# Kernel optimization log

Measured on AMD Instinct MI355X. Metric: run time of the kernel, lower is better.

## Reference

```python
import jax, jax.numpy as jnp
import numpy as np


def _prelu(x, a):
    return jnp.where(x >= 0, x, a * x)


def setup_inputs() -> dict:
    key = jax.random.key(0)
    ks = jax.random.split(key, 10)
    B, N, h_dim, H_dim, g_dim, Kc, n = 64, 4096, 256, 1024, 512, 32, 2048
    hs = jax.random.normal(ks[0], (B, N, h_dim), dtype=jnp.float32)
    cs_o = jax.random.randint(ks[1], (B, N), 0, Kc, dtype=jnp.int32)

    def lin(k, fi, fo):
        return jax.random.normal(k, (fi, fo), dtype=jnp.float32) / np.sqrt(fi).astype(np.float32)

    a = jnp.full((1,), 0.25, dtype=jnp.float32)  # torch PReLU default
    return {
        "hs": hs,
        "W1": lin(ks[2], h_dim, H_dim), "b1": jnp.zeros((H_dim,), jnp.float32), "a1": a,
        "W2": lin(ks[3], H_dim, H_dim), "b2": jnp.zeros((H_dim,), jnp.float32), "a2": a,
        "W3": lin(ks[4], H_dim, H_dim), "b3": jnp.zeros((H_dim,), jnp.float32), "a3": a,
        "W4": lin(ks[5], H_dim, H_dim), "b4": jnp.zeros((H_dim,), jnp.float32), "a4": a,
        "W5": lin(ks[6], H_dim, H_dim), "b5": jnp.zeros((H_dim,), jnp.float32), "a5": a,
        "W6": lin(ks[7], H_dim, g_dim), "b6": jnp.zeros((g_dim,), jnp.float32),
        "cs_o": cs_o,
        "n": n,
    }


def reference(hs, W1, b1, a1, W2, b2, a2, W3, b3, a3, W4, b4, a4, W5, b5, a5, W6, b6, cs_o, n):
    B, N, h_dim = hs.shape
    cs = cs_o.at[:, n:].set(-1)                  # points >= n are unassigned
    K = int(jnp.max(cs)) + 1                      # static (concrete data)
    Ks = jnp.max(cs, axis=1)                      # [B] max cluster id per batch entry

    # per-cluster masked sums (vectorized segment-sum over all K at once)
    onehot = (cs[:, :, None] == jnp.arange(K)[None, None, :]).astype(hs.dtype)  # [B,N,K]
    Hk = jnp.einsum('bnk,bnh->bkh', onehot, hs)   # [B,K,h] sum of hs per cluster
    hn = hs[:, n, :]                              # [B,h] the point being assigned
    # H = [H_0..H_{K-1}, H_0+h_n..H_{K-1}+h_n, h_n]
    H = jnp.concatenate([Hk, Hk + hn[:, None, :], hn[:, None, :]], axis=1)  # [B,2K+1,h]

    mk = (jnp.sum(onehot, axis=1) > 0).astype(hs.dtype)  # [B,K] cluster non-empty
    gs_mask = jnp.concatenate([mk, mk, jnp.ones((B, 1), hs.dtype)], axis=1)[:, :, None]

    # 6-layer MLP g applied to all B*(2K+1) rows at once
    x = H.reshape(B * (2 * K + 1), h_dim)
    x = _prelu(x @ W1 + b1, a1)
    x = _prelu(x @ W2 + b2, a2)
    x = _prelu(x @ W3 + b3, a3)
    x = _prelu(x @ W4 + b4, a4)
    x = _prelu(x @ W5 + b5, a5)
    gs = (x @ W6 + b6).reshape(B, 2 * K + 1, -1) * gs_mask  # [B,2K+1,g]

    # G_k = sum_{j<K, j!=k} gs_j + gs_{k+K} ;  G_K = sum_{j<K} gs_j + gs_{2K}
    S = jnp.sum(gs[:, :K], axis=1)                                   # [B,g]
    G_head = (S[:, None, :] - gs[:, :K] + gs[:, K:2 * K]) * mk[:, :, None]
    G_last = S + gs[:, 2 * K]
    G = jnp.concatenate([G_head, G_last[:, None, :]], axis=1)        # [B,K+1,g]

    # per-batch correction: if Ks[b]==k (k<K-1), move G[b,-1] to slot k+1, zero last
    need = (Ks >= 0) & (Ks < K - 1)
    kidx = jnp.arange(K + 1)
    move = need[:, None] & (kidx[None, :] == (Ks + 1)[:, None])      # [B,K+1]
    G = jnp.where(move[:, :, None], G[:, K:K + 1, :], G)
    G = jnp.where((need[:, None] & (kidx[None, :] == K))[:, :, None], 0.0, G)
    G_mask = jnp.where(need[:, None] & (kidx[None, :] >= (Ks + 2)[:, None]),
                       0.0, jnp.ones((B, K + 1), hs.dtype))
    return (G, G_mask)
```

## Files before the change

### kernel.cpp

```cpp
#include <hip/hip_runtime.h>
#include <hip/hip_bf16.h>
#include <stdint.h>

using bf16x8 = __attribute__((ext_vector_type(8))) short;
using f32x4  = __attribute__((ext_vector_type(4))) float;

#define BATCH 64
#define NTOK  4096
#define HD    256
#define HDIM  1024
#define GD    512

__device__ __forceinline__ ushort f2bf(float f) {
  union { __hip_bfloat16 h; ushort u; } cv;
  cv.h = __float2bfloat16(f);
  return cv.u;
}

__device__ __forceinline__ void gload_lds16(const void* gsrc, void* ldst) {
  typedef const __attribute__((address_space(1))) uint32_t* gas_p;
  typedef __attribute__((address_space(3))) uint32_t* las_p;
  __builtin_amdgcn_global_load_lds((gas_p)(uintptr_t)gsrc, (las_p)(uintptr_t)ldst, 16, 0, 0);
}

struct WTArgs {
  const float* src[6];
  ushort* dst[6];
  int fi[6];
  int fo[6];
};

__global__ __launch_bounds__(256) void wtrans_kernel(WTArgs a) {
  int z = blockIdx.z;
  int fi = a.fi[z], fo = a.fo[z];
  int c0 = blockIdx.x * 32;
  int r0 = blockIdx.y * 32;
  if (c0 >= fo || r0 >= fi) return;
  const float* W = a.src[z];
  ushort* Wt = a.dst[z];
  __shared__ float tile[32][33];
  int tx = threadIdx.x & 31, ty = threadIdx.x >> 5;
#pragma unroll
  for (int j = 0; j < 4; ++j)
    tile[ty + j * 8][tx] = W[(size_t)(r0 + ty + j * 8) * fo + (c0 + tx)];
  __syncthreads();
#pragma unroll
  for (int j = 0; j < 4; ++j)
    Wt[(size_t)(c0 + ty + j * 8) * fi + (r0 + tx)] = f2bf(tile[tx][ty + j * 8]);
}

__global__ __launch_bounds__(256) void bucket_kernel(const int* __restrict__ cs,
                                                     const int* __restrict__ nptr,
                                                     int* __restrict__ idx,
                                                     int* __restrict__ off,
                                                     int* __restrict__ cnt,
                                                     int* __restrict__ Ks,
                                                     int K) {
  int b = blockIdx.x, t = threadIdx.x;
  int n = *nptr;
  __shared__ int csb[NTOK];
  __shared__ int hist[256 * 32];
  __shared__ int btot[32];
  __shared__ int bbase[32];
  const int* csrow = cs + (size_t)b * NTOK;
  int mymax = -1;
  for (int i = t; i < n; i += 256) { int v = csrow[i]; csb[i] = v; mymax = max(mymax, v); }
#pragma unroll
  for (int k = 0; k < 32; ++k) hist[t * 32 + k] = 0;
  __syncthreads();
  int chunkN = (n + 255) >> 8;
  for (int c = 0; c < chunkN; ++c) {
    int i = c * 256 + t;
    if (i < n) hist[t * 32 + csb[i]]++;
  }
  __syncthreads();
  if (t < K) {
    int run = 0;
    for (int r = 0; r < 256; ++r) { int tmp = hist[r * 32 + t]; hist[r * 32 + t] = run; run += tmp; }
    btot[t] = run;
  }
  __syncthreads();
  if (t == 0) {
    int base = 0;
    for (int k = 0; k < K; ++k) { bbase[k] = base; base += btot[k]; }
  }
  __syncthreads();
  if (t < K) { off[b * K + t] = bbase[t]; cnt[b * K + t] = btot[t]; }
  int* idxb = idx + (size_t)b * NTOK;
  for (int c = 0; c < chunkN; ++c) {
    int i = c * 256 + t;
    if (i < n) {
      int k = csb[i];
      int s = bbase[k] + hist[t * 32 + k]++;
      idxb[s] = i;
    }
  }
  for (int o2 = 32; o2; o2 >>= 1) mymax = max(mymax, __shfl_down(mymax, o2));
  __shared__ int red[4];
  if ((t & 63) == 0) red[t >> 6] = mymax;
  __syncthreads();
  if (t == 0) {
    int r = red[0];
    for (int i = 1; i < 4; ++i) r = max(r, red[i]);
    Ks[b] = r;
  }
}

__global__ __launch_bounds__(256) void aggregate2_kernel(const float* __restrict__ hs,
                                                         const int* __restrict__ idx,
                                                         const int* __restrict__ off,
                                                         const int* __restrict__ cnt,
                                                         const int* __restrict__ nptr,
                                                         ushort* __restrict__ X,
                                                         int K) {
  int b = blockIdx.x / K, k = blockIdx.x % K;
  int t = threadIdx.x;
  int n = *nptr;
  int c = cnt[b * K + k];
  int o = off[b * K + k];
  const float* hsb = hs + (size_t)b * NTOK * HD;
  const int* ids = idx + (size_t)b * NTOK + o;
  __shared__ int sid[256];
  float a0 = 0.f, a1 = 0.f, a2 = 0.f, a3 = 0.f;
  for (int j0 = 0; j0 < c; j0 += 256) {
    __syncthreads();
    if (j0 + t < c) sid[t] = ids[j0 + t];
    __syncthreads();
    int lim = min(256, c - j0);
    int j = 0;
    for (; j + 3 < lim; j += 4) {
      int i0 = sid[j], i1 = sid[j + 1], i2 = sid[j + 2], i3 = sid[j + 3];
      a0 += hsb[(size_t)i0 * HD + t];
      a1 += hsb[(size_t)i1 * HD + t];
      a2 += hsb[(size_t)i2 * HD + t];
      a3 += hsb[(size_t)i3 * HD + t];
    }
    for (; j < lim; ++j) a0 += hsb[(size_t)sid[j] * HD + t];
  }
  float sum = (a0 + a1) + (a2 + a3);
  float hn = hsb[(size_t)n * HD + t];
  int R = 2 * K + 1;
  X[((size_t)b * R + k) * HD + t]     = f2bf(sum);
  X[((size_t)b * R + K + k) * HD + t] = f2bf(sum + hn);
  if (k == 0) X[((size_t)b * R + 2 * K) * HD + t] = f2bf(hn);
}

template <bool LAST>
__global__ __launch_bounds__(256) void gemm_kernel(const ushort* __restrict__ A,
                                                   const ushort* __restrict__ Bt,
                                                   const float* __restrict__ bias,
                                                   const float* __restrict__ aptr,
                                                   void* __restrict__ Cout,
                                                   int N, int Kd) {
  __shared__ ushort As[2][2][128 * 32];
  __shared__ ushort Bs[2][2][64 * 32];
  int tid = threadIdx.x;
  int lane = tid & 63, w = tid >> 6;
  int wr = w >> 1, wc = w & 1;
  int fr = lane & 15, fq = lane >> 4;

  int nwg = gridDim.x;
  int flat = blockIdx.x;
  int q8 = nwg >> 3, r8 = nwg & 7;
  int xcd = flat & 7, loc = flat >> 3;
  int swz = (xcd < r8 ? xcd * (q8 + 1) : r8 * (q8 + 1) + (xcd - r8) * q8) + loc;
  int NC = N >> 6;
  int brow = swz / NC, bcol = swz % NC;

  size_t row0 = (size_t)brow * 128;
  size_t col0 = (size_t)bcol * 64;

  const ushort* Abase = A + row0 * (size_t)Kd;
  const ushort* Bbase = Bt + col0 * (size_t)Kd;

  f32x4 acc[4][2] = {};

  int qA0 = w * 64 + lane;
  int qA1 = 256 + w * 64 + lane;
  int rA0 = qA0 >> 2, kA0 = (qA0 & 3) * 8;
  int rA1 = qA1 >> 2, kA1 = (qA1 & 3) * 8;
  int rB = qA0 >> 2, kB = (qA0 & 3) * 8;

  auto stage = [&](int buf, int k0) {
#pragma unroll
    for (int h = 0; h < 2; ++h) {
      int kh = k0 + h * 32;
      gload_lds16(Abase + (size_t)rA0 * Kd + kh + kA0, &As[buf][h][(w)     * 512]);
      gload_lds16(Abase + (size_t)rA1 * Kd + kh + kA1, &As[buf][h][(4 + w) * 512]);
      gload_lds16(Bbase + (size_t)rB  * Kd + kh + kB,  &Bs[buf][h][(w)     * 512]);
    }
  };

  int nt = Kd >> 6;
  int cur = 0;
  stage(0, 0);
  __syncthreads();
  for (int t = 0; t < nt; ++t) {
    if (t + 1 < nt) stage(cur ^ 1, (t + 1) * 64);
    bf16x8 af[2][4], bfv[2][2];
#pragma unroll
    for (int h = 0; h < 2; ++h) {
#pragma unroll
      for (int m = 0; m < 4; ++m)
        af[h][m] = *(const bf16x8*)&As[cur][h][(wr * 64 + m * 16 + fr) * 32 + fq * 8];
#pragma unroll
      for (int nn = 0; nn < 2; ++nn)
        bfv[h][nn] = *(const bf16x8*)&Bs[cur][h][(wc * 32 + nn * 16 + fr) * 32 + fq * 8];
    }
#pragma unroll
    for (int h = 0; h < 2; ++h)
#pragma unroll
      for (int m = 0; m < 4; ++m)
#pragma unroll
        for (int nn = 0; nn < 2; ++nn)
          acc[m][nn] = __builtin_amdgcn_mfma_f32_16x16x32_bf16(af[h][m], bfv[h][nn], acc[m][nn], 0, 0, 0);
    __syncthreads();
    cur ^= 1;
  }

  float alpha = 0.f;
  if (!LAST) alpha = aptr[0];
#pragma unroll
  for (int nn = 0; nn < 2; ++nn) {
    size_t col = col0 + wc * 32 + nn * 16 + fr;
    float bv = bias[col];
#pragma unroll
    for (int m = 0; m < 4; ++m) {
      size_t rbase = row0 + wr * 64 + m * 16 + fq * 4;
#pragma unroll
      for (int j = 0; j < 4; ++j) {
        float v = acc[m][nn][j] + bv;
        if (!LAST) {
          v = (v >= 0.f) ? v : alpha * v;
          ((ushort*)Cout)[(rbase + j) * N + col] = f2bf(v);
        } else {
          ((float*)Cout)[(rbase + j) * N + col] = v;
        }
      }
    }
  }
}

__global__ __launch_bounds__(256) void final_kernel(const float* __restrict__ gs,
                                                    const int* __restrict__ counts,
                                                    const int* __restrict__ Ks,
                                                    float* __restrict__ out,
                                                    int K) {
  int b = blockIdx.x, t = threadIdx.x;
  __shared__ float mk[64];
  __shared__ int sks;
  if (t < K) mk[t] = (counts[b * K + t] > 0) ? 1.f : 0.f;
  if (t == 0) sks = Ks[b];
  __syncthreads();
  int ks = sks;
  bool need = (ks >= 0) && (ks < K - 1);
  const float* g = gs + (size_t)b * (2 * K + 1) * GD;
  float S0 = 0.f, S1 = 0.f;
  for (int k = 0; k < K; ++k) {
    S0 += g[(size_t)k * GD + t] * mk[k];
    S1 += g[(size_t)k * GD + t + 256] * mk[k];
  }
  float gl0 = S0 + g[(size_t)(2 * K) * GD + t];
  float gl1 = S1 + g[(size_t)(2 * K) * GD + t + 256];
  float* G  = out + (size_t)b * (K + 1) * GD;
  float* Gm = out + (size_t)BATCH * (K + 1) * GD + (size_t)b * (K + 1);
  for (int kk = 0; kk <= K; ++kk) {
    float v0, v1;
    if (kk == K)                  { v0 = need ? 0.f : gl0; v1 = need ? 0.f : gl1; }
    else if (need && kk == ks + 1){ v0 = gl0;              v1 = gl1; }
    else {
      v0 = mk[kk] * (S0 - g[(size_t)kk * GD + t]       + g[(size_t)(K + kk) * GD + t]);
      v1 = mk[kk] * (S1 - g[(size_t)kk * GD + t + 256] + g[(size_t)(K + kk) * GD + t + 256]);
    }
    G[(size_t)kk * GD + t]       = v0;
    G[(size_t)kk * GD + t + 256] = v1;
  }
  if (t <= K) Gm[t] = (need && t >= ks + 2) ? 0.f : 1.f;
}

extern "C" void kernel_launch(void* const* d_in, const int* in_sizes, int n_in,
                              void* d_out, int out_size, void* d_ws, size_t ws_size,
                              hipStream_t stream) {
  const float* hs = (const float*)d_in[0];
  const float* W[6]  = {(const float*)d_in[1], (const float*)d_in[4], (const float*)d_in[7],
                        (const float*)d_in[10], (const float*)d_in[13], (const float*)d_in[16]};
  const float* bb[6] = {(const float*)d_in[2], (const float*)d_in[5], (const float*)d_in[8],
                        (const float*)d_in[11], (const float*)d_in[14], (const float*)d_in[17]};
  const float* aa[5] = {(const float*)d_in[3], (const float*)d_in[6], (const float*)d_in[9],
                        (const float*)d_in[12], (const float*)d_in[15]};
  const int* cs   = (const int*)d_in[18];
  const int* nptr = (const int*)d_in[19];
  float* out = (float*)d_out;

  int K = out_size / (BATCH * (GD + 1)) - 1;
  int M = BATCH * (2 * K + 1);
  int Mpad = (M + 127) / 128 * 128;

  char* base = (char*)d_ws;
  size_t off_b = 0;
  auto alloc = [&](size_t bytes) {
    char* p = base + off_b;
    off_b = (off_b + bytes + 255) & ~(size_t)255;
    return p;
  };
  ushort* W1t  = (ushort*)alloc((size_t)HDIM * HD * 2);
  ushort* W2t  = (ushort*)alloc((size_t)HDIM * HDIM * 2);
  ushort* W3t  = (ushort*)alloc((size_t)HDIM * HDIM * 2);
  ushort* W4t  = (ushort*)alloc((size_t)HDIM * HDIM * 2);
  ushort* W5bt = (ushort*)alloc((size_t)HDIM * HDIM * 2);
  ushort* W6t  = (ushort*)alloc((size_t)GD * HDIM * 2);
  int* idx     = (int*)alloc((size_t)BATCH * NTOK * 4);
  int* offb    = (int*)alloc((size_t)BATCH * K * 4);
  int* cntb    = (int*)alloc((size_t)BATCH * K * 4);
  int* Ksb     = (int*)alloc(BATCH * 4);
  ushort* X    = (ushort*)alloc((size_t)Mpad * HD * 2);
  ushort* Y0   = (ushort*)alloc((size_t)Mpad * HDIM * 2);
  ushort* Y1   = (ushort*)alloc((size_t)Mpad * HDIM * 2);
  float*  gsb  = (float*)alloc((size_t)Mpad * GD * 4);
  (void)ws_size; (void)n_in; (void)in_sizes;

  WTArgs wa;
  wa.src[0] = W[0]; wa.dst[0] = W1t;  wa.fi[0] = HD;   wa.fo[0] = HDIM;
  wa.src[1] = W[1]; wa.dst[1] = W2t;  wa.fi[1] = HDIM; wa.fo[1] = HDIM;
  wa.src[2] = W[2]; wa.dst[2] = W3t;  wa.fi[2] = HDIM; wa.fo[2] = HDIM;
  wa.src[3] = W[3]; wa.dst[3] = W4t;  wa.fi[3] = HDIM; wa.fo[3] = HDIM;
  wa.src[4] = W[4]; wa.dst[4] = W5bt; wa.fi[4] = HDIM; wa.fo[4] = HDIM;
  wa.src[5] = W[5]; wa.dst[5] = W6t;  wa.fi[5] = HDIM; wa.fo[5] = GD;
  hipLaunchKernelGGL(wtrans_kernel, dim3(32, 32, 6), dim3(256), 0, stream, wa);

  hipLaunchKernelGGL(bucket_kernel, dim3(BATCH), dim3(256), 0, stream, cs, nptr, idx, offb, cntb, Ksb, K);
  hipLaunchKernelGGL(aggregate2_kernel, dim3(BATCH * K), dim3(256), 0, stream, hs, idx, offb, cntb, nptr, X, K);
  hipMemsetAsync(X + (size_t)M * HD, 0, (size_t)(Mpad - M) * HD * 2, stream);

  dim3 blk(256);
  int NR = Mpad / 128;
  hipLaunchKernelGGL((gemm_kernel<false>), dim3(NR * (HDIM / 64)), blk, 0, stream, X,   W1t,  bb[0], aa[0], (void*)Y0, HDIM, HD);
  hipLaunchKernelGGL((gemm_kernel<false>), dim3(NR * (HDIM / 64)), blk, 0, stream, Y0,  W2t,  bb[1], aa[1], (void*)Y1, HDIM, HDIM);
  hipLaunchKernelGGL((gemm_kernel<false>), dim3(NR * (HDIM / 64)), blk, 0, stream, Y1,  W3t,  bb[2], aa[2], (void*)Y0, HDIM, HDIM);
  hipLaunchKernelGGL((gemm_kernel<false>), dim3(NR * (HDIM / 64)), blk, 0, stream, Y0,  W4t,  bb[3], aa[3], (void*)Y1, HDIM, HDIM);
  hipLaunchKernelGGL((gemm_kernel<false>), dim3(NR * (HDIM / 64)), blk, 0, stream, Y1,  W5bt, bb[4], aa[4], (void*)Y0, HDIM, HDIM);
  hipLaunchKernelGGL((gemm_kernel<true>),  dim3(NR * (GD / 64)),   blk, 0, stream, Y0,  W6t,  bb[5], nullptr, (void*)gsb, GD, HDIM);

  hipLaunchKernelGGL(final_kernel, dim3(BATCH), dim3(256), 0, stream, gsb, cntb, Ksb, out, K);
}
```

Measured before the change: 155.4 us.

## Merge preprocessing kernels, vectorize aggregation, triple-buffer GEMM with single barrier

Combines the weight transpose and bucketing into one launch with a flat grid, removing a kernel launch and the wasted empty blocks of the 3D transpose grid. The aggregation kernel now reads float4 rows split across four wavefronts and reduces the partials in shared memory, and it zeroes the padding rows itself so the separate memset goes away. The GEMM moves to a 3-stage LDS ring with explicit vmcnt waits, one barrier per k-step and raised priority around the MFMA block, so global loads are issued two steps ahead. This raises LDS use per GEMM block, which may reduce occupancy.

```diff
diff --git a/kernel.cpp b/kernel.cpp
--- a/kernel.cpp
+++ b/kernel.cpp
@@ -30,79 +30,86 @@
   int fo[6];
 };
 
-__global__ __launch_bounds__(256) void wtrans_kernel(WTArgs a) {
-  int z = blockIdx.z;
-  int fi = a.fi[z], fo = a.fo[z];
-  int c0 = blockIdx.x * 32;
-  int r0 = blockIdx.y * 32;
-  if (c0 >= fo || r0 >= fi) return;
-  const float* W = a.src[z];
-  ushort* Wt = a.dst[z];
-  __shared__ float tile[32][33];
-  int tx = threadIdx.x & 31, ty = threadIdx.x >> 5;
-#pragma unroll
-  for (int j = 0; j < 4; ++j)
-    tile[ty + j * 8][tx] = W[(size_t)(r0 + ty + j * 8) * fo + (c0 + tx)];
-  __syncthreads();
-#pragma unroll
-  for (int j = 0; j < 4; ++j)
-    Wt[(size_t)(c0 + ty + j * 8) * fi + (r0 + tx)] = f2bf(tile[tx][ty + j * 8]);
-}
-
-__global__ __launch_bounds__(256) void bucket_kernel(const int* __restrict__ cs,
-                                                     const int* __restrict__ nptr,
-                                                     int* __restrict__ idx,
-                                                     int* __restrict__ off,
-                                                     int* __restrict__ cnt,
-                                                     int* __restrict__ Ks,
-                                                     int K) {
-  int b = blockIdx.x, t = threadIdx.x;
-  int n = *nptr;
+__global__ __launch_bounds__(256) void pre_kernel(WTArgs a,
+                                                  const int* __restrict__ cs,
+                                                  const int* __restrict__ nptr,
+                                                  int* __restrict__ idx,
+                                                  int* __restrict__ off,
+                                                  int* __restrict__ cnt,
+                                                  int* __restrict__ Ks,
+                                                  int K) {
   __shared__ int csb[NTOK];
   __shared__ int hist[256 * 32];
   __shared__ int btot[32];
   __shared__ int bbase[32];
-  const int* csrow = cs + (size_t)b * NTOK;
-  int mymax = -1;
-  for (int i = t; i < n; i += 256) { int v = csrow[i]; csb[i] = v; mymax = max(mymax, v); }
-#pragma unroll
-  for (int k = 0; k < 32; ++k) hist[t * 32 + k] = 0;
-  __syncthreads();
-  int chunkN = (n + 255) >> 8;
-  for (int c = 0; c < chunkN; ++c) {
-    int i = c * 256 + t;
-    if (i < n) hist[t * 32 + csb[i]]++;
-  }
-  __syncthreads();
-  if (t < K) {
-    int run = 0;
-    for (int r = 0; r < 256; ++r) { int tmp = hist[r * 32 + t]; hist[r * 32 + t] = run; run += tmp; }
-    btot[t] = run;
-  }
-  __syncthreads();
-  if (t == 0) {
-    int base = 0;
-    for (int k = 0; k < K; ++k) { bbase[k] = base; base += btot[k]; }
-  }
-  __syncthreads();
-  if (t < K) { off[b * K + t] = bbase[t]; cnt[b * K + t] = btot[t]; }
-  int* idxb = idx + (size_t)b * NTOK;
-  for (int c = 0; c < chunkN; ++c) {
-    int i = c * 256 + t;
-    if (i < n) {
-      int k = csb[i];
-      int s = bbase[k] + hist[t * 32 + k]++;
-      idxb[s] = i;
-    }
-  }
-  for (int o2 = 32; o2; o2 >>= 1) mymax = max(mymax, __shfl_down(mymax, o2));
-  __shared__ int red[4];
-  if ((t & 63) == 0) red[t >> 6] = mymax;
-  __syncthreads();
-  if (t == 0) {
-    int r = red[0];
-    for (int i = 1; i < 4; ++i) r = max(r, red[i]);
-    Ks[b] = r;
+  __shared__ float tile[32][33];
+  int t = threadIdx.x;
+  if (blockIdx.x < BATCH) {
+    int b = blockIdx.x;
+    int n = *nptr;
+    const int* csrow = cs + (size_t)b * NTOK;
+    int mymax = -1;
+    for (int i = t; i < n; i += 256) { int v = csrow[i]; csb[i] = v; mymax = max(mymax, v); }
+#pragma unroll
+    for (int k = 0; k < 32; ++k) hist[t * 32 + k] = 0;
+    __syncthreads();
+    int chunkN = (n + 255) >> 8;
+    for (int c = 0; c < chunkN; ++c) {
+      int i = c * 256 + t;
+      if (i < n) hist[t * 32 + csb[i]]++;
+    }
+    __syncthreads();
+    if (t < K) {
+      int run = 0;
+      for (int r = 0; r < 256; ++r) { int tmp = hist[r * 32 + t]; hist[r * 32 + t] = run; run += tmp; }
+      btot[t] = run;
+    }
+    __syncthreads();
+    if (t == 0) {
+      int base = 0;
+      for (int k = 0; k < K; ++k) { bbase[k] = base; base += btot[k]; }
+    }
+    __syncthreads();
+    if (t < K) { off[b * K + t] = bbase[t]; cnt[b * K + t] = btot[t]; }
+    int* idxb = idx + (size_t)b * NTOK;
+    for (int c = 0; c < chunkN; ++c) {
+      int i = c * 256 + t;
+      if (i < n) {
+        int k = csb[i];
+        int s = bbase[k] + hist[t * 32 + k]++;
+        idxb[s] = i;
+      }
+    }
+    for (int o2 = 32; o2; o2 >>= 1) mymax = max(mymax, __shfl_down(mymax, o2));
+    if ((t & 63) == 0) btot[16 + (t >> 6)] = mymax;
+    __syncthreads();
+    if (t == 0) {
+      int r = btot[16];
+      for (int i = 1; i < 4; ++i) r = max(r, btot[16 + i]);
+      Ks[b] = r;
+    }
+  } else {
+    int f = blockIdx.x - BATCH;
+    int z = 0;
+    while (true) {
+      int nb = (a.fo[z] >> 5) * (a.fi[z] >> 5);
+      if (f < nb) break;
+      f -= nb; ++z;
+    }
+    int ncx = a.fo[z] >> 5;
+    int cx = f % ncx, cy = f / ncx;
+    int c0 = cx * 32, r0 = cy * 32;
+    int fo = a.fo[z], fi = a.fi[z];
+    const float* W = a.src[z];
+    ushort* Wt = a.dst[z];
+    int tx = t & 31, ty = t >> 5;
+#pragma unroll
+    for (int j = 0; j < 4; ++j)
+      tile[ty + j * 8][tx] = W[(size_t)(r0 + ty + j * 8) * fo + (c0 + tx)];
+    __syncthreads();
+#pragma unroll
+    for (int j = 0; j < 4; ++j)
+      Wt[(size_t)(c0 + ty + j * 8) * fi + (r0 + tx)] = f2bf(tile[tx][ty + j * 8]);
   }
 }
 
@@ -112,37 +119,50 @@
                                                          const int* __restrict__ cnt,
                                                          const int* __restrict__ nptr,
                                                          ushort* __restrict__ X,
-                                                         int K) {
+                                                         int K, int M, int Mpad) {
   int b = blockIdx.x / K, k = blockIdx.x % K;
   int t = threadIdx.x;
+  int g = t >> 6, l = t & 63;
   int n = *nptr;
   int c = cnt[b * K + k];
   int o = off[b * K + k];
   const float* hsb = hs + (size_t)b * NTOK * HD;
   const int* ids = idx + (size_t)b * NTOK + o;
   __shared__ int sid[256];
-  float a0 = 0.f, a1 = 0.f, a2 = 0.f, a3 = 0.f;
+  __shared__ float part[4][HD];
+  float ax = 0.f, ay = 0.f, az = 0.f, aw = 0.f;
+  float bx = 0.f, by = 0.f, bz = 0.f, bw = 0.f;
   for (int j0 = 0; j0 < c; j0 += 256) {
     __syncthreads();
     if (j0 + t < c) sid[t] = ids[j0 + t];
     __syncthreads();
     int lim = min(256, c - j0);
-    int j = 0;
-    for (; j + 3 < lim; j += 4) {
-      int i0 = sid[j], i1 = sid[j + 1], i2 = sid[j + 2], i3 = sid[j + 3];
-      a0 += hsb[(size_t)i0 * HD + t];
-      a1 += hsb[(size_t)i1 * HD + t];
-      a2 += hsb[(size_t)i2 * HD + t];
-      a3 += hsb[(size_t)i3 * HD + t];
-    }
-    for (; j < lim; ++j) a0 += hsb[(size_t)sid[j] * HD + t];
-  }
-  float sum = (a0 + a1) + (a2 + a3);
+    int j = g;
+    for (; j + 4 < lim; j += 8) {
+      float4 v0 = ((const float4*)&hsb[(size_t)sid[j] * HD])[l];
+      float4 v1 = ((const float4*)&hsb[(size_t)sid[j + 4] * HD])[l];
+      ax += v0.x; ay += v0.y; az += v0.z; aw += v0.w;
+      bx += v1.x; by += v1.y; bz += v1.z; bw += v1.w;
+    }
+    for (; j < lim; j += 4) {
+      float4 v = ((const float4*)&hsb[(size_t)sid[j] * HD])[l];
+      ax += v.x; ay += v.y; az += v.z; aw += v.w;
+    }
+  }
+  part[g][l * 4 + 0] = ax + bx;
+  part[g][l * 4 + 1] = ay + by;
+  part[g][l * 4 + 2] = az + bz;
+  part[g][l * 4 + 3] = aw + bw;
+  __syncthreads();
+  float sum = ((part[0][t] + part[1][t]) + (part[2][t] + part[3][t]));
   float hn = hsb[(size_t)n * HD + t];
   int R = 2 * K + 1;
   X[((size_t)b * R + k) * HD + t]     = f2bf(sum);
   X[((size_t)b * R + K + k) * HD + t] = f2bf(sum + hn);
-  if (k == 0) X[((size_t)b * R + 2 * K) * HD + t] = f2bf(hn);
+  if (k == 0) {
+    X[((size_t)b * R + 2 * K) * HD + t] = f2bf(hn);
+    for (int r = M + b; r < Mpad; r += BATCH) X[(size_t)r * HD + t] = 0;
+  }
 }
 
 template <bool LAST>
@@ -152,8 +172,8 @@
                                                    const float* __restrict__ aptr,
                                                    void* __restrict__ Cout,
                                                    int N, int Kd) {
-  __shared__ ushort As[2][2][128 * 32];
-  __shared__ ushort Bs[2][2][64 * 32];
+  __shared__ ushort As[3][2][128 * 32];
+  __shared__ ushort Bs[3][2][64 * 32];
   int tid = threadIdx.x;
   int lane = tid & 63, w = tid >> 6;
   int wr = w >> 1, wc = w & 1;
@@ -192,11 +212,14 @@
   };
 
   int nt = Kd >> 6;
-  int cur = 0;
   stage(0, 0);
-  __syncthreads();
+  stage(1, 64);
   for (int t = 0; t < nt; ++t) {
-    if (t + 1 < nt) stage(cur ^ 1, (t + 1) * 64);
+    if (t + 1 < nt) asm volatile("s_waitcnt vmcnt(6)" ::: "memory");
+    else            asm volatile("s_waitcnt vmcnt(0)" ::: "memory");
+    __builtin_amdgcn_s_barrier();
+    __builtin_amdgcn_sched_barrier(0);
+    int cur = t % 3;
     bf16x8 af[2][4], bfv[2][2];
 #pragma unroll
     for (int h = 0; h < 2; ++h) {
@@ -207,6 +230,7 @@
       for (int nn = 0; nn < 2; ++nn)
         bfv[h][nn] = *(const bf16x8*)&Bs[cur][h][(wc * 32 + nn * 16 + fr) * 32 + fq * 8];
     }
+    __builtin_amdgcn_s_setprio(1);
 #pragma unroll
     for (int h = 0; h < 2; ++h)
 #pragma unroll
@@ -214,8 +238,8 @@
 #pragma unroll
         for (int nn = 0; nn < 2; ++nn)
           acc[m][nn] = __builtin_amdgcn_mfma_f32_16x16x32_bf16(af[h][m], bfv[h][nn], acc[m][nn], 0, 0, 0);
-    __syncthreads();
-    cur ^= 1;
+    __builtin_amdgcn_s_setprio(0);
+    if (t + 2 < nt) stage((t + 2) % 3, (t + 2) * 64);
   }
 
   float alpha = 0.f;
@@ -326,11 +350,13 @@
   wa.src[3] = W[3]; wa.dst[3] = W4t;  wa.fi[3] = HDIM; wa.fo[3] = HDIM;
   wa.src[4] = W[4]; wa.dst[4] = W5bt; wa.fi[4] = HDIM; wa.fo[4] = HDIM;
   wa.src[5] = W[5]; wa.dst[5] = W6t;  wa.fi[5] = HDIM; wa.fo[5] = GD;
-  hipLaunchKernelGGL(wtrans_kernel, dim3(32, 32, 6), dim3(256), 0, stream, wa);
-
-  hipLaunchKernelGGL(bucket_kernel, dim3(BATCH), dim3(256), 0, stream, cs, nptr, idx, offb, cntb, Ksb, K);
-  hipLaunchKernelGGL(aggregate2_kernel, dim3(BATCH * K), dim3(256), 0, stream, hs, idx, offb, cntb, nptr, X, K);
-  hipMemsetAsync(X + (size_t)M * HD, 0, (size_t)(Mpad - M) * HD * 2, stream);
+  int nbw = 0;
+  for (int z = 0; z < 6; ++z) nbw += (wa.fo[z] / 32) * (wa.fi[z] / 32);
+  hipLaunchKernelGGL(pre_kernel, dim3(BATCH + nbw), dim3(256), 0, stream,
+                     wa, cs, nptr, idx, offb, cntb, Ksb, K);
+
+  hipLaunchKernelGGL(aggregate2_kernel, dim3(BATCH * K), dim3(256), 0, stream,
+                     hs, idx, offb, cntb, nptr, X, K, M, Mpad);
 
   dim3 blk(256);
   int NR = Mpad / 128;
```

New measurement: 166.8 us. +7.3%, slower.
